# Kernel optimization log

Measured on AMD Instinct MI355X. Metric: run time of the kernel, lower is better.

Reference implementation:

```python
import jax, jax.numpy as jnp
import numpy as np

B, S, DIM, H = 2, 2048, 1536, 12
HD = DIM // H  # 128
EPS = 1e-6


def setup_inputs() -> dict:
    key = jax.random.key(0)
    ks = jax.random.split(key, 6)
    x = jax.random.normal(ks[0], (B, S, DIM), dtype=jnp.float32)
    # RoPE rotation as (cos, sin) pairs: shape [S, 1, HD//2, 2]
    inv = 1.0 / (10000.0 ** (np.arange(0, HD, 2, dtype=np.float32) / HD))
    ang = np.arange(S, dtype=np.float32)[:, None] * inv[None, :]  # [S, HD//2]
    freqs = jnp.asarray(np.stack([np.cos(ang), np.sin(ang)], axis=-1))[:, None, :, :]
    def lin(k):
        return jax.random.normal(k, (DIM, DIM), dtype=jnp.float32) * 0.02
    wq, wk, wv, wo = lin(ks[1]), lin(ks[2]), lin(ks[3]), lin(ks[4])
    zb = jnp.zeros((DIM,), dtype=jnp.float32)
    ones = jnp.ones((DIM,), dtype=jnp.float32)
    return dict(x=x, freqs=freqs,
                wq=wq, bq=zb, wk=wk, bk=zb, wv=wv, bv=zb, wo=wo, bo=zb,
                gq=ones, gk=ones, timestep=500)


def reference(x, freqs, wq, bq, wk, bk, wv, bv, wo, bo, gq, gk, timestep):
    b, s, dim = x.shape

    def rms(z, g):
        zf = z.astype(jnp.float32)
        n = zf * jax.lax.rsqrt(jnp.mean(zf * zf, axis=-1, keepdims=True) + EPS)
        return n.astype(z.dtype) * g

    def rope(t):
        # [b,s,dim] -> [b,s,H,HD//2,2] pairs; complex multiply by freqs
        tp = t.reshape(b, s, H, HD // 2, 2)
        tr, ti = tp[..., 0], tp[..., 1]
        fr = freqs[None, ..., 0]  # [1,s,1,HD//2] broadcasts over batch & heads
        fi = freqs[None, ..., 1]
        out = jnp.stack([tr * fr - ti * fi, tr * fi + ti * fr], axis=-1)
        return out.reshape(b, s, dim)

    q = rope(rms(x @ wq.T + bq, gq))
    k = rope(rms(x @ wk.T + bk, gk))
    v = x @ wv.T + bv

    qh = q.reshape(b, s, H, HD).transpose(0, 2, 1, 3)
    kh = k.reshape(b, s, H, HD).transpose(0, 2, 1, 3)
    vh = v.reshape(b, s, H, HD).transpose(0, 2, 1, 3)
    scores = jnp.einsum('bhqd,bhkd->bhqk', qh, kh) / np.float32(np.sqrt(HD))
    attn = jax.nn.softmax(scores, axis=-1)
    out = jnp.einsum('bhqk,bhkd->bhqd', attn, vh)
    out = out.transpose(0, 2, 1, 3).reshape(b, s, dim)
    return out @ wo.T + bo
```

## Files before the change

kernel.cpp:

```cpp
#include <hip/hip_runtime.h>
#include <hip/hip_bf16.h>


#define BQ  2
#define SQ  2048
#define DIMQ 1536
#define HQ  12
#define HDQ 128
#define MTOK 4096
#define KDIM 1536

typedef __attribute__((ext_vector_type(8))) short short8;
typedef __attribute__((ext_vector_type(4))) float f32x4;
typedef __attribute__((ext_vector_type(16))) float f32x16;
typedef __attribute__((ext_vector_type(8))) unsigned short u16x8;

typedef __attribute__((address_space(1))) const void global_cvoid;
typedef __attribute__((address_space(3))) void lds_void;

__device__ __forceinline__ float bf2f(unsigned int u) {
    return __uint_as_float(u << 16);
}
__device__ __forceinline__ unsigned short f2bf(float f) {
    unsigned int u = __float_as_uint(f);
    u += 0x7fffu + ((u >> 16) & 1u);
    return (unsigned short)(u >> 16);
}
__device__ __forceinline__ void gload_lds16(const void* g, void* l) {
    __builtin_amdgcn_global_load_lds((global_cvoid*)g, (lds_void*)l, 16, 0, 0);
}
__device__ __forceinline__ unsigned int cvtpk_bf16(float lo, float hi) {
    unsigned int r;
    asm("v_cvt_pk_bf16_f32 %0, %1, %2" : "=v"(r) : "v"(lo), "v"(hi));
    return r;
}

__global__ __launch_bounds__(256)
void cast_f32_bf16(const float* __restrict__ src, unsigned short* __restrict__ dst, int n4) {
    int i = blockIdx.x * blockDim.x + threadIdx.x;
    int stride = gridDim.x * blockDim.x;
    for (; i < n4; i += stride) {
        float4 v = ((const float4*)src)[i];
        unsigned short a = f2bf(v.x), b = f2bf(v.y), c = f2bf(v.z), d = f2bf(v.w);
        unsigned int lo = (unsigned int)a | ((unsigned int)b << 16);
        unsigned int hi = (unsigned int)c | ((unsigned int)d << 16);
        ((uint2*)dst)[i] = make_uint2(lo, hi);
    }
}

template<int MODE>
__global__ __launch_bounds__(256)
void gemm_bt(const unsigned short* __restrict__ A,
             const unsigned short* __restrict__ Bm,
             unsigned short* __restrict__ oQ,
             unsigned short* __restrict__ oK,
             unsigned short* __restrict__ oV,
             const float* __restrict__ biasq,
             const float* __restrict__ biask,
             const float* __restrict__ biasv,
             float* __restrict__ oF,
             const float* __restrict__ biaso)
{
    __shared__ unsigned short ldsA[128 * 64];
    __shared__ unsigned short ldsB[128 * 64];
    const int m0 = blockIdx.x * 128;
    const int n0 = blockIdx.y * 128;
    const int t = threadIdx.x;
    const int lane = t & 63;
    const int wid = t >> 6;
    const int wr = (wid >> 1) * 64;
    const int wc = (wid & 1) * 64;
    const int lr = lane & 15;
    const int lk = lane >> 4;

    f32x4 acc[4][4] = {};

    #pragma unroll 1
    for (int kt = 0; kt < KDIM; kt += 64) {
        #pragma unroll
        for (int i = 0; i < 4; ++i) {
            const int off = i * 4096 + wid * 1024 + lane * 16;
            const int r = off >> 7;
            const int c = (off >> 4) & 7;
            const int csw = (c ^ (r & 7)) << 3;
            gload_lds16(A + (size_t)(m0 + r) * KDIM + kt + csw,
                        (char*)ldsA + i * 4096 + wid * 1024);
            gload_lds16(Bm + (size_t)(n0 + r) * KDIM + kt + csw,
                        (char*)ldsB + i * 4096 + wid * 1024);
        }
        __syncthreads();

        #pragma unroll
        for (int kk = 0; kk < 2; ++kk) {
            short8 af[4], bf[4];
            #pragma unroll
            for (int mi = 0; mi < 4; ++mi) {
                int row = wr + mi * 16 + lr;
                int ch = (kk * 4 + lk) ^ (row & 7);
                af[mi] = *(const short8*)((const char*)ldsA + row * 128 + ch * 16);
            }
            #pragma unroll
            for (int ni = 0; ni < 4; ++ni) {
                int row = wc + ni * 16 + lr;
                int ch = (kk * 4 + lk) ^ (row & 7);
                bf[ni] = *(const short8*)((const char*)ldsB + row * 128 + ch * 16);
            }
            #pragma unroll
            for (int mi = 0; mi < 4; ++mi)
                #pragma unroll
                for (int ni = 0; ni < 4; ++ni)
                    acc[mi][ni] = __builtin_amdgcn_mfma_f32_16x16x32_bf16(
                        af[mi], bf[ni], acc[mi][ni], 0, 0, 0);
        }
        __syncthreads();
    }

    if (MODE == 0) {
        const int seg = n0 / 1536;
        unsigned short* op = (seg == 0) ? oQ : (seg == 1 ? oK : oV);
        const float* bp = (seg == 0) ? biasq : (seg == 1 ? biask : biasv);
        const int nl0 = n0 - seg * 1536;
        #pragma unroll
        for (int mi = 0; mi < 4; ++mi)
            #pragma unroll
            for (int ni = 0; ni < 4; ++ni)
                #pragma unroll
                for (int j = 0; j < 4; ++j) {
                    int row = m0 + wr + mi * 16 + lk * 4 + j;
                    int col = nl0 + wc + ni * 16 + lr;
                    op[(size_t)row * 1536 + col] = f2bf(acc[mi][ni][j] + bp[col]);
                }
    } else {
        #pragma unroll
        for (int mi = 0; mi < 4; ++mi)
            #pragma unroll
            for (int ni = 0; ni < 4; ++ni)
                #pragma unroll
                for (int j = 0; j < 4; ++j) {
                    int row = m0 + wr + mi * 16 + lk * 4 + j;
                    int col = n0 + wc + ni * 16 + lr;
                    oF[(size_t)row * 1536 + col] = acc[mi][ni][j] + biaso[col];
                }
    }
}

__global__ __launch_bounds__(256)
void rmsnorm_rope(unsigned short* __restrict__ T,
                  const float* __restrict__ g,
                  const float* __restrict__ freqs)
{
    const int token = blockIdx.x;
    const int s = token & (SQ - 1);
    unsigned int* row = (unsigned int*)(T + (size_t)token * DIMQ);
    const int t = threadIdx.x;
    const int lane = t & 63, wid = t >> 6;

    float pr[3], pi[3];
    float ss = 0.f;
    #pragma unroll
    for (int q = 0; q < 3; ++q) {
        unsigned int v = row[t + q * 256];
        float a = bf2f(v & 0xffffu);
        float b = bf2f(v >> 16);
        pr[q] = a; pi[q] = b;
        ss += a * a + b * b;
    }
    ss += __shfl_xor(ss, 32); ss += __shfl_xor(ss, 16); ss += __shfl_xor(ss, 8);
    ss += __shfl_xor(ss, 4);  ss += __shfl_xor(ss, 2);  ss += __shfl_xor(ss, 1);
    __shared__ float red[4];
    if (lane == 0) red[wid] = ss;
    __syncthreads();
    float tot = red[0] + red[1] + red[2] + red[3];
    float sc = rsqrtf(tot * (1.0f / 1536.0f) + 1e-6f);

    #pragma unroll
    for (int q = 0; q < 3; ++q) {
        int p = t + q * 256;
        int ph = p & 63;
        float fr = freqs[s * 128 + ph * 2];
        float fi = freqs[s * 128 + ph * 2 + 1];
        float nr = pr[q] * sc * g[2 * p];
        float ni = pi[q] * sc * g[2 * p + 1];
        float outr = nr * fr - ni * fi;
        float outi = nr * fi + ni * fr;
        row[p] = (unsigned int)f2bf(outr) | ((unsigned int)f2bf(outi) << 16);
    }
}

__global__ __launch_bounds__(256)
void vtrans(const unsigned short* __restrict__ V, unsigned short* __restrict__ Vt)
{
    __shared__ unsigned short tile[64][72];
    const int s0 = blockIdx.x * 64;
    const int d0 = blockIdx.y * 64;
    const int bh = blockIdx.z;
    const int b = bh / HQ, h = bh % HQ;
    const int t = threadIdx.x;

    #pragma unroll
    for (int i = 0; i < 2; ++i) {
        int cid = i * 256 + t;
        int r = cid >> 3, c = cid & 7;
        u16x8 v = *(const u16x8*)(V + (size_t)(b * SQ + s0 + r) * DIMQ + h * HDQ + d0 + c * 8);
        #pragma unroll
        for (int e = 0; e < 8; ++e) tile[r][c * 8 + e] = v[e];
    }
    __syncthreads();
    #pragma unroll
    for (int i = 0; i < 2; ++i) {
        int cid = i * 256 + t;
        int rd = cid >> 3, c = cid & 7;
        u16x8 w;
        #pragma unroll
        for (int e = 0; e < 8; ++e) w[e] = tile[c * 8 + e][rd];
        *(u16x8*)(Vt + (size_t)(bh * HDQ + d0 + rd) * SQ + s0 + c * 8) = w;
    }
}

__global__ __launch_bounds__(128)
void attn(const unsigned short* __restrict__ Q,
          const unsigned short* __restrict__ Kb,
          const unsigned short* __restrict__ Vt,
          unsigned short* __restrict__ Ao)
{
    __shared__ char smem[32768];
    char* Kl = smem;
    char* Vl = smem + 16384;

    const int fid = blockIdx.x;
    const int xcd = fid & 7;
    const int slot = fid >> 3;
    const int bh = xcd * 3 + (slot >> 5);
    const int sblk = slot & 31;
    const int b = bh / HQ, h = bh % HQ;
    const int s0 = sblk * 64;

    const int t = threadIdx.x;
    const int lane = t & 63, wid = t >> 6;
    const int l31 = lane & 31, hi = lane >> 5;
    const float scale = 0.08838834764831845f;
    const float THR = 90.5f;

    short8 qf[8];
    {
        const int qrow = b * SQ + s0 + wid * 32 + l31;
        const unsigned short* qp = Q + (size_t)qrow * DIMQ + h * HDQ;
        #pragma unroll
        for (int kc = 0; kc < 8; ++kc)
            qf[kc] = *(const short8*)(qp + kc * 16 + hi * 8);
    }

    float mrun = -1e30f, lsum = 0.f;
    f32x16 oacc[4] = {};

    const unsigned short* Kbase = Kb + (size_t)(b * SQ) * DIMQ + h * HDQ;
    const unsigned short* Vbase = Vt + (size_t)(bh * HDQ) * SQ;

    #pragma unroll 1
    for (int kv0 = 0; kv0 < SQ; kv0 += 64) {
        #pragma unroll
        for (int i = 0; i < 8; ++i) {
            const int off = i * 2048 + t * 16;
            {
                int r = off >> 8;
                int c = (off >> 4) & 15;
                gload_lds16(Kbase + (size_t)(kv0 + r) * DIMQ + ((c ^ (r & 7)) << 3),
                            Kl + i * 2048 + wid * 1024);
            }
            {
                int r = off >> 7;
                int c = (off >> 4) & 7;
                gload_lds16(Vbase + (size_t)r * SQ + kv0 + ((c ^ (r & 7)) << 3),
                            Vl + i * 2048 + wid * 1024);
            }
        }
        __syncthreads();

        f32x16 sacc[2] = {};
        #pragma unroll
        for (int kvt = 0; kvt < 2; ++kvt) {
            const int krow = kvt * 32 + l31;
            const int rb = krow * 256;
            #pragma unroll
            for (int kc = 0; kc < 8; ++kc) {
                int ch = (kc * 2 + hi) ^ (krow & 7);
                short8 kf = *(const short8*)(Kl + rb + ch * 16);
                sacc[kvt] = __builtin_amdgcn_mfma_f32_32x32x16_bf16(kf, qf[kc], sacc[kvt], 0, 0, 0);
            }
        }

        float tm = sacc[0][0];
        #pragma unroll
        for (int r = 1; r < 16; ++r) tm = fmaxf(tm, sacc[0][r]);
        #pragma unroll
        for (int r = 0; r < 16; ++r) tm = fmaxf(tm, sacc[1][r]);
        tm = fmaxf(tm, __shfl_xor(tm, 32));
        if (!__all(tm <= mrun + THR)) {
            float mnew = fmaxf(mrun, tm);
            float al = __expf((mrun - mnew) * scale);
            lsum *= al;
            #pragma unroll
            for (int dt = 0; dt < 4; ++dt)
                #pragma unroll
                for (int r = 0; r < 16; ++r) oacc[dt][r] *= al;
            mrun = mnew;
        }
        float rs = 0.f;
        #pragma unroll
        for (int kvt = 0; kvt < 2; ++kvt)
            #pragma unroll
            for (int r = 0; r < 16; ++r) {
                float p = __expf((sacc[kvt][r] - mrun) * scale);
                sacc[kvt][r] = p;
                rs += p;
            }
        rs += __shfl_xor(rs, 32);
        lsum += rs;

        #pragma unroll
        for (int ks = 0; ks < 4; ++ks) {
            const int g = ks * 8;
            #define SV(f) (sacc[(f) >> 4][(f) & 15])
            unsigned int a0 = cvtpk_bf16(SV(g + 0), SV(g + 1));
            unsigned int a1 = cvtpk_bf16(SV(g + 2), SV(g + 3));
            unsigned int b0 = cvtpk_bf16(SV(g + 4), SV(g + 5));
            unsigned int b1 = cvtpk_bf16(SV(g + 6), SV(g + 7));
            #undef SV
            unsigned int xa0 = __shfl_xor(a0, 32);
            unsigned int xa1 = __shfl_xor(a1, 32);
            unsigned int xb0 = __shfl_xor(b0, 32);
            unsigned int xb1 = __shfl_xor(b1, 32);
            union { unsigned int w[4]; short8 v; } pf;
            pf.w[0] = hi ? xb0 : a0;
            pf.w[1] = hi ? xb1 : a1;
            pf.w[2] = hi ? b0 : xa0;
            pf.w[3] = hi ? b1 : xa1;
            #pragma unroll
            for (int dt = 0; dt < 4; ++dt) {
                const int drow = dt * 32 + l31;
                int ch = (ks * 2 + hi) ^ (drow & 7);
                short8 vf = *(const short8*)(Vl + drow * 128 + ch * 16);
                oacc[dt] = __builtin_amdgcn_mfma_f32_32x32x16_bf16(vf, pf.v, oacc[dt], 0, 0, 0);
            }
        }
        __syncthreads();
    }

    const float rls = 1.0f / lsum;
    char* Ot = smem + wid * 8192;
    #pragma unroll
    for (int dt = 0; dt < 4; ++dt)
        #pragma unroll
        for (int rp = 0; rp < 8; ++rp) {
            const int r = 2 * rp;
            float v0 = oacc[dt][r] * rls;
            float v1 = oacc[dt][r + 1] * rls;
            int d = dt * 32 + (r & 3) + 8 * (r >> 2) + 4 * hi;
            unsigned int w = (unsigned int)f2bf(v0) | ((unsigned int)f2bf(v1) << 16);
            int addr = l31 * 256 + (((d >> 3) ^ (l31 & 7)) << 4) + (d & 7) * 2;
            *(unsigned int*)(Ot + addr) = w;
        }
    #pragma unroll
    for (int ii = 0; ii < 8; ++ii) {
        int task = ii * 64 + lane;
        int q = task >> 4, c = task & 15;
        u16x8 vv = *(const u16x8*)(Ot + q * 256 + ((c ^ (q & 7)) << 4));
        int tok = b * SQ + s0 + wid * 32 + q;
        *(u16x8*)(Ao + (size_t)tok * DIMQ + h * HDQ + c * 8) = vv;
    }
}

extern "C" void kernel_launch(void* const* d_in, const int* in_sizes, int n_in,
                              void* d_out, int out_size, void* d_ws, size_t ws_size,
                              hipStream_t stream) {
    (void)in_sizes; (void)n_in; (void)out_size; (void)ws_size;
    const float* x     = (const float*)d_in[0];
    const float* freqs = (const float*)d_in[1];
    const float* wq = (const float*)d_in[2];
    const float* bq = (const float*)d_in[3];
    const float* wk = (const float*)d_in[4];
    const float* bk = (const float*)d_in[5];
    const float* wv = (const float*)d_in[6];
    const float* bv = (const float*)d_in[7];
    const float* wo = (const float*)d_in[8];
    const float* bo = (const float*)d_in[9];
    const float* gq = (const float*)d_in[10];
    const float* gk = (const float*)d_in[11];
    float* out = (float*)d_out;

    char* w = (char*)d_ws;
    unsigned short* Xb   = (unsigned short*)(w);
    unsigned short* Wqkv = (unsigned short*)(w + 12582912);
    unsigned short* Wob  = (unsigned short*)(w + 26738688);
    unsigned short* Qb   = (unsigned short*)(w + 31457280);
    unsigned short* Kbuf = (unsigned short*)(w + 44040192);
    unsigned short* Vb   = (unsigned short*)(w + 56623104);
    unsigned short* Vt   = (unsigned short*)(w + 69206016);
    unsigned short* Ao   = Xb;

    cast_f32_bf16<<<2048, 256, 0, stream>>>(x,  Xb,            6291456 / 4);
    cast_f32_bf16<<<1024, 256, 0, stream>>>(wq, Wqkv,          2359296 / 4);
    cast_f32_bf16<<<1024, 256, 0, stream>>>(wk, Wqkv + 2359296, 2359296 / 4);
    cast_f32_bf16<<<1024, 256, 0, stream>>>(wv, Wqkv + 4718592, 2359296 / 4);
    cast_f32_bf16<<<1024, 256, 0, stream>>>(wo, Wob,           2359296 / 4);

    gemm_bt<0><<<dim3(32, 36), 256, 0, stream>>>(
        Xb, Wqkv, Qb, Kbuf, Vb, bq, bk, bv, nullptr, nullptr);

    rmsnorm_rope<<<4096, 256, 0, stream>>>(Qb,   gq, freqs);
    rmsnorm_rope<<<4096, 256, 0, stream>>>(Kbuf, gk, freqs);
    vtrans<<<dim3(32, 2, 24), 256, 0, stream>>>(Vb, Vt);

    attn<<<768, 128, 0, stream>>>(Qb, Kbuf, Vt, Ao);

    gemm_bt<1><<<dim3(32, 12), 256, 0, stream>>>(
        Ao, Wob, nullptr, nullptr, nullptr, nullptr, nullptr, nullptr, out, bo);
}
```

Measured before the change: 283.4 us.

## Double-buffer K tiles in attention, use exp2 softmax, fuse cast kernels

The attention kernel now double-buffers K tiles in LDS, prefetching the next K block while computing the current one. It replaces the block-wide syncthreads with vmcnt waits and barriers so V loads overlap the QK^T and softmax work. Softmax uses exp2 with a prescaled constant and a tree max reduction, and MFMA sections run at raised wave priority. The five separate f32-to-bf16 cast launches are merged into one kernel; the extra LDS use (48KB) may reduce attention occupancy.

```diff
diff --git a/kernel.cpp b/kernel.cpp
--- a/kernel.cpp
+++ b/kernel.cpp
@@ -35,16 +35,37 @@
     return r;
 }
 
+#define VMCNT(n) asm volatile("s_waitcnt vmcnt(" #n ")" ::: "memory")
+#define BARRIER() do { asm volatile("" ::: "memory"); \
+                       __builtin_amdgcn_s_barrier();  \
+                       asm volatile("" ::: "memory"); } while (0)
+
 __global__ __launch_bounds__(256)
-void cast_f32_bf16(const float* __restrict__ src, unsigned short* __restrict__ dst, int n4) {
+void cast_all(const float* __restrict__ x,
+              const float* __restrict__ wq, const float* __restrict__ wk,
+              const float* __restrict__ wv, const float* __restrict__ wo,
+              unsigned short* __restrict__ Xb,
+              unsigned short* __restrict__ Wqkv,
+              unsigned short* __restrict__ Wob)
+{
+    const int NX = 1572864, NW = 589824;
     int i = blockIdx.x * blockDim.x + threadIdx.x;
     int stride = gridDim.x * blockDim.x;
-    for (; i < n4; i += stride) {
-        float4 v = ((const float4*)src)[i];
-        unsigned short a = f2bf(v.x), b = f2bf(v.y), c = f2bf(v.z), d = f2bf(v.w);
+    for (; i < NX + 4 * NW; i += stride) {
+        const float* s; unsigned short* d; int off;
+        if (i < NX) { s = x; d = Xb; off = i; }
+        else {
+            int j = i - NX;
+            int seg = j / NW;
+            off = j - seg * NW;
+            s = (seg == 0) ? wq : (seg == 1) ? wk : (seg == 2) ? wv : wo;
+            d = (seg < 3) ? (Wqkv + seg * 2359296) : Wob;
+        }
+        float4 v = ((const float4*)s)[off];
+        unsigned short a = f2bf(v.x), b = f2bf(v.y), c = f2bf(v.z), e = f2bf(v.w);
         unsigned int lo = (unsigned int)a | ((unsigned int)b << 16);
-        unsigned int hi = (unsigned int)c | ((unsigned int)d << 16);
-        ((uint2*)dst)[i] = make_uint2(lo, hi);
+        unsigned int hi = (unsigned int)c | ((unsigned int)e << 16);
+        ((uint2*)d)[off] = make_uint2(lo, hi);
     }
 }
 
@@ -223,9 +244,10 @@
           const unsigned short* __restrict__ Vt,
           unsigned short* __restrict__ Ao)
 {
-    __shared__ char smem[32768];
-    char* Kl = smem;
-    char* Vl = smem + 16384;
+    __shared__ char smem[49152];
+    char* Kl0 = smem;
+    char* Kl1 = smem + 16384;
+    char* Vl  = smem + 32768;
 
     const int fid = blockIdx.x;
     const int xcd = fid & 7;
@@ -238,8 +260,11 @@
     const int t = threadIdx.x;
     const int lane = t & 63, wid = t >> 6;
     const int l31 = lane & 31, hi = lane >> 5;
-    const float scale = 0.08838834764831845f;
     const float THR = 90.5f;
+    const float CE = 0.12751879f;
+
+    const unsigned short* Kbase = Kb + (size_t)(b * SQ) * DIMQ + h * HDQ;
+    const unsigned short* Vbase = Vt + (size_t)(bh * HDQ) * SQ;
 
     short8 qf[8];
     {
@@ -253,30 +278,41 @@
     float mrun = -1e30f, lsum = 0.f;
     f32x16 oacc[4] = {};
 
-    const unsigned short* Kbase = Kb + (size_t)(b * SQ) * DIMQ + h * HDQ;
-    const unsigned short* Vbase = Vt + (size_t)(bh * HDQ) * SQ;
+    #pragma unroll
+    for (int i = 0; i < 8; ++i) {
+        const int off = i * 2048 + t * 16;
+        int r = off >> 8, c = (off >> 4) & 15;
+        gload_lds16(Kbase + (size_t)r * DIMQ + ((c ^ (r & 7)) << 3),
+                    Kl0 + i * 2048 + wid * 1024);
+    }
+
+    char* kcur = Kl0;
+    char* knxt = Kl1;
 
     #pragma unroll 1
     for (int kv0 = 0; kv0 < SQ; kv0 += 64) {
         #pragma unroll
         for (int i = 0; i < 8; ++i) {
             const int off = i * 2048 + t * 16;
-            {
-                int r = off >> 8;
-                int c = (off >> 4) & 15;
-                gload_lds16(Kbase + (size_t)(kv0 + r) * DIMQ + ((c ^ (r & 7)) << 3),
-                            Kl + i * 2048 + wid * 1024);
-            }
-            {
-                int r = off >> 7;
-                int c = (off >> 4) & 7;
-                gload_lds16(Vbase + (size_t)r * SQ + kv0 + ((c ^ (r & 7)) << 3),
-                            Vl + i * 2048 + wid * 1024);
-            }
-        }
-        __syncthreads();
+            int r = off >> 7, c = (off >> 4) & 7;
+            gload_lds16(Vbase + (size_t)r * SQ + kv0 + ((c ^ (r & 7)) << 3),
+                        Vl + i * 2048 + wid * 1024);
+        }
+        asm volatile("" ::: "memory");
+        const int kvn = (kv0 + 64 < SQ) ? kv0 + 64 : kv0;
+        #pragma unroll
+        for (int i = 0; i < 8; ++i) {
+            const int off = i * 2048 + t * 16;
+            int r = off >> 8, c = (off >> 4) & 15;
+            gload_lds16(Kbase + (size_t)(kvn + r) * DIMQ + ((c ^ (r & 7)) << 3),
+                        knxt + i * 2048 + wid * 1024);
+        }
+
+        VMCNT(16);
+        BARRIER();
 
         f32x16 sacc[2] = {};
+        __builtin_amdgcn_s_setprio(1);
         #pragma unroll
         for (int kvt = 0; kvt < 2; ++kvt) {
             const int krow = kvt * 32 + l31;
@@ -284,20 +320,25 @@
             #pragma unroll
             for (int kc = 0; kc < 8; ++kc) {
                 int ch = (kc * 2 + hi) ^ (krow & 7);
-                short8 kf = *(const short8*)(Kl + rb + ch * 16);
+                short8 kf = *(const short8*)(kcur + rb + ch * 16);
                 sacc[kvt] = __builtin_amdgcn_mfma_f32_32x32x16_bf16(kf, qf[kc], sacc[kvt], 0, 0, 0);
             }
         }
-
-        float tm = sacc[0][0];
-        #pragma unroll
-        for (int r = 1; r < 16; ++r) tm = fmaxf(tm, sacc[0][r]);
-        #pragma unroll
-        for (int r = 0; r < 16; ++r) tm = fmaxf(tm, sacc[1][r]);
+        __builtin_amdgcn_s_setprio(0);
+
+        float mt[16];
+        #pragma unroll
+        for (int r = 0; r < 16; ++r) mt[r] = fmaxf(sacc[0][r], sacc[1][r]);
+        #pragma unroll
+        for (int s = 8; s > 0; s >>= 1)
+            #pragma unroll
+            for (int r = 0; r < 8; ++r)
+                if (r < s) mt[r] = fmaxf(mt[r], mt[r + s]);
+        float tm = mt[0];
         tm = fmaxf(tm, __shfl_xor(tm, 32));
         if (!__all(tm <= mrun + THR)) {
             float mnew = fmaxf(mrun, tm);
-            float al = __expf((mrun - mnew) * scale);
+            float al = __builtin_amdgcn_exp2f((mrun - mnew) * CE);
             lsum *= al;
             #pragma unroll
             for (int dt = 0; dt < 4; ++dt)
@@ -310,13 +351,17 @@
         for (int kvt = 0; kvt < 2; ++kvt)
             #pragma unroll
             for (int r = 0; r < 16; ++r) {
-                float p = __expf((sacc[kvt][r] - mrun) * scale);
+                float p = __builtin_amdgcn_exp2f((sacc[kvt][r] - mrun) * CE);
                 sacc[kvt][r] = p;
                 rs += p;
             }
         rs += __shfl_xor(rs, 32);
         lsum += rs;
 
+        VMCNT(8);
+        BARRIER();
+
+        __builtin_amdgcn_s_setprio(1);
         #pragma unroll
         for (int ks = 0; ks < 4; ++ks) {
             const int g = ks * 8;
@@ -343,11 +388,15 @@
                 oacc[dt] = __builtin_amdgcn_mfma_f32_32x32x16_bf16(vf, pf.v, oacc[dt], 0, 0, 0);
             }
         }
-        __syncthreads();
+        __builtin_amdgcn_s_setprio(0);
+
+        BARRIER();
+
+        char* tmp = kcur; kcur = knxt; knxt = tmp;
     }
 
     const float rls = 1.0f / lsum;
-    char* Ot = smem + wid * 8192;
+    char* Ot = smem + 32768 + wid * 8192;
     #pragma unroll
     for (int dt = 0; dt < 4; ++dt)
         #pragma unroll
@@ -398,11 +447,7 @@
     unsigned short* Vt   = (unsigned short*)(w + 69206016);
     unsigned short* Ao   = Xb;
 
-    cast_f32_bf16<<<2048, 256, 0, stream>>>(x,  Xb,            6291456 / 4);
-    cast_f32_bf16<<<1024, 256, 0, stream>>>(wq, Wqkv,          2359296 / 4);
-    cast_f32_bf16<<<1024, 256, 0, stream>>>(wk, Wqkv + 2359296, 2359296 / 4);
-    cast_f32_bf16<<<1024, 256, 0, stream>>>(wv, Wqkv + 4718592, 2359296 / 4);
-    cast_f32_bf16<<<1024, 256, 0, stream>>>(wo, Wob,           2359296 / 4);
+    cast_all<<<2048, 256, 0, stream>>>(x, wq, wk, wv, wo, Xb, Wqkv, Wob);
 
     gemm_bt<0><<<dim3(32, 36), 256, 0, stream>>>(
         Xb, Wqkv, Qb, Kbuf, Vb, bq, bk, bv, nullptr, nullptr);
```

Measured after the change: 277.9 us. No clear change (-1.9%).
